# Performance work log

Hardware: AMD Instinct MI355X
Metric: run time of the kernel (lower is better)

## Reference

```python
import jax, jax.numpy as jnp
import numpy as np
import math

GROUPS = 32
EPS = 1e-5
NUM_HEADS = 8


def group_norm(x, gamma, beta):
    # x: [B, C, H, W]; normalize within each of GROUPS channel groups over (C/G, H, W)
    B, C, H, W = x.shape
    xg = x.reshape(B, GROUPS, C // GROUPS, H, W)
    mean = jnp.mean(xg, axis=(2, 3, 4), keepdims=True)
    var = jnp.var(xg, axis=(2, 3, 4), keepdims=True)
    xn = ((xg - mean) * jax.lax.rsqrt(var + EPS)).reshape(B, C, H, W)
    return xn * gamma[None, :, None, None] + beta[None, :, None, None]


def setup_inputs() -> dict:
    key = jax.random.key(0)
    ks = jax.random.split(key, 10)
    C = 512
    B, H, W = 2, 64, 64
    s = 1.0 / math.sqrt(C)
    return {
        "x": jax.random.normal(ks[0], (B, C, H, W), jnp.float32),
        "gamma": jnp.ones((C,), jnp.float32),
        "beta": jnp.zeros((C,), jnp.float32),
        "Wq": jax.random.normal(ks[1], (C, C), jnp.float32) * s,
        "bq": jax.random.normal(ks[2], (C,), jnp.float32) * 0.01,
        "Wk": jax.random.normal(ks[3], (C, C), jnp.float32) * s,
        "bk": jax.random.normal(ks[4], (C,), jnp.float32) * 0.01,
        "Wv": jax.random.normal(ks[5], (C, C), jnp.float32) * s,
        "bv": jax.random.normal(ks[6], (C,), jnp.float32) * 0.01,
        "Wo": jax.random.normal(ks[7], (C, C), jnp.float32) * s,
        "bo": jax.random.normal(ks[8], (C,), jnp.float32) * 0.01,
    }


def reference(x, gamma, beta, Wq, bq, Wk, bk, Wv, bv, Wo, bo):
    B, C, H, W = x.shape
    N = H * W
    hd = C // NUM_HEADS
    h = group_norm(x, gamma, beta)
    h = h.reshape(B, C, N).transpose(0, 2, 1)  # [B, N, C]
    # torch nn.Linear: y = x @ W.T + b
    q = (h @ Wq.T + bq).reshape(B, N, NUM_HEADS, hd)
    k = (h @ Wk.T + bk).reshape(B, N, NUM_HEADS, hd)
    v = (h @ Wv.T + bv).reshape(B, N, NUM_HEADS, hd)
    scale = 1.0 / math.sqrt(hd)
    attn = jnp.einsum('bihd,bjhd->bijh', q, k) * scale  # [B, N, N, heads]
    attn = jax.nn.softmax(attn, axis=2)
    o = jnp.einsum('bijh,bjhd->bihd', attn, v).reshape(B, N, C)
    o = o @ Wo.T + bo
    o = o.transpose(0, 2, 1).reshape(B, C, H, W)
    return x + o
```

## Files before the change

### kernel.cpp

```cpp
#include <hip/hip_runtime.h>
#include <cstdint>
#include <cstddef>

typedef __bf16 bf16x8 __attribute__((ext_vector_type(8)));
typedef float f32x4 __attribute__((ext_vector_type(4)));
typedef float f32x16 __attribute__((ext_vector_type(16)));
typedef unsigned short ushort8 __attribute__((ext_vector_type(8)));
typedef unsigned u32x2 __attribute__((ext_vector_type(2)));
typedef float f4 __attribute__((ext_vector_type(4)));

__device__ __forceinline__ unsigned short f2bf(float f) {
    __bf16 b = (__bf16)f;
    return *(unsigned short*)&b;
}
__device__ __forceinline__ unsigned pk2bf(float a, float b) {
    __bf16 x = (__bf16)a, y = (__bf16)b;
    unsigned short ux = *(unsigned short*)&x, uy = *(unsigned short*)&y;
    return (unsigned)ux | ((unsigned)uy << 16);
}
__device__ __forceinline__ float bf2f(unsigned short u) {
    union { unsigned u; float f; } v; v.u = ((unsigned)u) << 16; return v.f;
}

#if __has_builtin(__builtin_amdgcn_exp2f)
#define EXP2(x) __builtin_amdgcn_exp2f(x)
#else
#define EXP2(x) exp2f(x)
#endif

__device__ __forceinline__ void pl32swap(unsigned& x, unsigned& y) {
#if __has_builtin(__builtin_amdgcn_permlane32_swap)
    auto r = __builtin_amdgcn_permlane32_swap(x, y, false, false);
    x = r[0]; y = r[1];
#else
    unsigned xs = (unsigned)__shfl_xor((int)x, 32, 64);
    unsigned ys = (unsigned)__shfl_xor((int)y, 32, 64);
    bool lo = ((threadIdx.x & 63) < 32);
    unsigned nx = lo ? x : ys;
    unsigned ny = lo ? xs : y;
    x = nx; y = ny;
#endif
}

#define GLL(g, l) __builtin_amdgcn_global_load_lds( \
    (__attribute__((address_space(1))) void*)(g), \
    (__attribute__((address_space(3))) void*)(l), 16, 0, 0)

#define CS 0.18033688011112042f
#define SPLITS 2

__global__ __launch_bounds__(256) void prep(
    const float* __restrict__ wq, const float* __restrict__ wk,
    const float* __restrict__ wv, const float* __restrict__ wo,
    unsigned short* __restrict__ wb,
    const float* __restrict__ x, float* __restrict__ part)
{
    const int bid = blockIdx.x;
    if (bid < 4096) {
        int i = bid * 256 + threadIdx.x;
        const float* src = (i < 262144) ? wq : (i < 524288) ? wk : (i < 786432) ? wv : wo;
        wb[i] = f2bf(src[i & 262143]);
        return;
    }
    const int blk = bid - 4096;
    const int q = blk & 3, bg = blk >> 2;
    const f4* xv = (const f4*)(x + (size_t)bg * 65536 + q * 16384);
    float s = 0.f, sq = 0.f;
    for (int i = threadIdx.x; i < 4096; i += 256) {
        f4 v = xv[i];
        s  += v.x + v.y + v.z + v.w;
        sq += v.x * v.x + v.y * v.y + v.z * v.z + v.w * v.w;
    }
    #pragma unroll
    for (int off = 32; off > 0; off >>= 1) {
        s  += __shfl_xor(s, off, 64);
        sq += __shfl_xor(sq, off, 64);
    }
    __shared__ float red[8];
    const int w = threadIdx.x >> 6, lane = threadIdx.x & 63;
    if (lane == 0) { red[w] = s; red[4 + w] = sq; }
    __syncthreads();
    if (threadIdx.x == 0) {
        part[(bg * 4 + q) * 2]     = red[0] + red[1] + red[2] + red[3];
        part[(bg * 4 + q) * 2 + 1] = red[4] + red[5] + red[6] + red[7];
    }
}

__global__ __launch_bounds__(256) void gn_apply(
    const float* __restrict__ x, const float* __restrict__ gamma,
    const float* __restrict__ beta, const float* __restrict__ part,
    unsigned short* __restrict__ h)
{
    const int q = blockIdx.x, bg = blockIdx.y;
    const int b = bg >> 5, g = bg & 31;
    float s = 0.f, sq = 0.f;
    #pragma unroll
    for (int j = 0; j < 4; ++j) {
        s  += part[(bg * 4 + j) * 2];
        sq += part[(bg * 4 + j) * 2 + 1];
    }
    const float mean = s * (1.f / 65536.f);
    const float rstd = rsqrtf(sq * (1.f / 65536.f) - mean * mean + 1e-5f);

    float gm[16], bt[16];
    #pragma unroll
    for (int c = 0; c < 16; ++c) {
        gm[c] = gamma[g * 16 + c] * rstd;
        bt[c] = beta[g * 16 + c];
    }
    const float* xg = x + (size_t)bg * 65536;
    const int n0 = q * 1024 + threadIdx.x * 4;
    float val[16][4];
    #pragma unroll
    for (int c = 0; c < 16; ++c) {
        f4 v = *(const f4*)&xg[(size_t)c * 4096 + n0];
        val[c][0] = (v.x - mean) * gm[c] + bt[c];
        val[c][1] = (v.y - mean) * gm[c] + bt[c];
        val[c][2] = (v.z - mean) * gm[c] + bt[c];
        val[c][3] = (v.w - mean) * gm[c] + bt[c];
    }
    #pragma unroll
    for (int nn = 0; nn < 4; ++nn) {
        ushort8 v0, v1;
        #pragma unroll
        for (int c = 0; c < 8; ++c)  v0[c]     = f2bf(val[c][nn]);
        #pragma unroll
        for (int c = 8; c < 16; ++c) v1[c - 8] = f2bf(val[c][nn]);
        unsigned short* dst = h + ((size_t)(b * 4096 + n0 + nn)) * 512 + g * 16;
        *(ushort8*)dst = v0;
        *(ushort8*)(dst + 8) = v1;
    }
}

__global__ __launch_bounds__(512, 2) void gemm_qkv(
    const unsigned short* __restrict__ A,
    const unsigned short* __restrict__ Bt,
    const float* __restrict__ bias0,
    const float* __restrict__ bias1,
    const float* __restrict__ bias2,
    unsigned short* __restrict__ outB,
    unsigned short* __restrict__ vtout)
{
    __shared__ __attribute__((aligned(16))) unsigned short As[128 * 32];
    __shared__ __attribute__((aligned(16))) unsigned short Bs[128 * 32];
    const int t = threadIdx.x;
    const int w = t >> 6, lane = t & 63;
    const int l15 = lane & 15, l4 = lane >> 4;
    const int bm = blockIdx.y, bn = blockIdx.x;
    const int wm = (w >> 2) * 64, wn = (w & 3) * 32;

    f32x4 acc[4][2] = {};

    const int srow = t >> 2, sc8 = (t & 3) * 8;
    const unsigned short* gA = A  + (size_t)(bm * 128 + srow) * 512 + sc8;
    const unsigned short* gB = Bt + (size_t)(bn * 128 + srow) * 512 + sc8;
    unsigned short* lA = &As[t * 8];
    unsigned short* lB = &Bs[t * 8];

    for (int k0 = 0; k0 < 512; k0 += 32) {
        __syncthreads();
        GLL(gA + k0, lA);
        GLL(gB + k0, lB);
        __syncthreads();

        bf16x8 af[4], bfr[2];
        #pragma unroll
        for (int mt = 0; mt < 4; ++mt)
            af[mt] = *(const bf16x8*)&As[(wm + mt * 16 + l15) * 32 + l4 * 8];
        #pragma unroll
        for (int nt = 0; nt < 2; ++nt)
            bfr[nt] = *(const bf16x8*)&Bs[(wn + nt * 16 + l15) * 32 + l4 * 8];
        #pragma unroll
        for (int mt = 0; mt < 4; ++mt)
            #pragma unroll
            for (int nt = 0; nt < 2; ++nt)
                acc[mt][nt] = __builtin_amdgcn_mfma_f32_16x16x32_bf16(
                    af[mt], bfr[nt], acc[mt][nt], 0, 0, 0);
    }

    #pragma unroll
    for (int nt = 0; nt < 2; ++nt) {
        int col = bn * 128 + wn + nt * 16 + l15;
        const float* bp = (col < 512) ? bias0 : (col < 1024) ? bias1 : bias2;
        float bv = bp[col & 511];
        if (col < 1024) {
            float sc = (col < 512) ? CS : 1.0f;
            #pragma unroll
            for (int mt = 0; mt < 4; ++mt)
                #pragma unroll
                for (int r = 0; r < 4; ++r) {
                    int row = bm * 128 + wm + mt * 16 + l4 * 4 + r;
                    outB[(size_t)row * 1024 + col] = f2bf((acc[mt][nt][r] + bv) * sc);
                }
        } else {
            int hd = col - 1024;
            #pragma unroll
            for (int mt = 0; mt < 4; ++mt) {
                int m = bm * 128 + wm + mt * 16 + l4 * 4;
                int bb = m >> 12, n = m & 4095;
                unsigned u0 = pk2bf(acc[mt][nt][0] + bv, acc[mt][nt][1] + bv);
                unsigned u1 = pk2bf(acc[mt][nt][2] + bv, acc[mt][nt][3] + bv);
                unsigned short* dst = vtout +
                    ((size_t)(bb * 8 + (hd >> 6)) * 64 + (hd & 63)) * 4096 + n;
                *(u32x2*)dst = (u32x2){u0, u1};
            }
        }
    }
}

__global__ __launch_bounds__(512, 2) void gemm_out(
    const unsigned short* __restrict__ A,
    const unsigned short* __restrict__ opart,
    const float* __restrict__ lbuf,
    const float* __restrict__ bias,
    const float* __restrict__ resid,
    float* __restrict__ outF)
{
    __shared__ __attribute__((aligned(16))) unsigned short As[128 * 32];
    __shared__ __attribute__((aligned(16))) unsigned short Bs[128 * 32];
    const int t = threadIdx.x;
    const int w = t >> 6, lane = t & 63;
    const int l15 = lane & 15, l4 = lane >> 4;
    const int bm = blockIdx.y, bn = blockIdx.x;
    const int wm = (w >> 2) * 64, wn = (w & 3) * 32;

    f32x4 acc[4][2] = {};

    const int srow = t >> 2, sc8 = (t & 3) * 8;
    const unsigned short* gA = A + (size_t)(bm * 128 + srow) * 512 + sc8;
    unsigned short* lA = &As[t * 8];
    unsigned short* lB = &Bs[t * 8];

    const int m = bn * 128 + srow;
    const int bb = m >> 12, q = m & 4095;
    const size_t prow0 = (size_t)(bb * 8) * 4096 + q;
    float inv[8];
    #pragma unroll
    for (int hh = 0; hh < 8; ++hh) {
        size_t pr = prow0 + (size_t)hh * 4096;
        inv[hh] = 1.f / (lbuf[pr] + lbuf[65536 + pr]);
    }
    const unsigned short* gO0 = opart + prow0 * 64;
    const unsigned short* gO1 = gO0 + (size_t)65536 * 64;

    ushort8 o0 = *(const ushort8*)(gO0 + sc8);
    ushort8 o1 = *(const ushort8*)(gO1 + sc8);

    for (int k0 = 0; k0 < 512; k0 += 32) {
        float iv = inv[k0 >> 6];
        ushort8 bv8;
        #pragma unroll
        for (int i = 0; i < 8; ++i)
            bv8[i] = f2bf((bf2f(o0[i]) + bf2f(o1[i])) * iv);
        if (k0 < 480) {
            size_t noff = (size_t)((k0 + 32) >> 6) * 262144 + ((k0 + 32) & 32) + sc8;
            o0 = *(const ushort8*)(gO0 + noff);
            o1 = *(const ushort8*)(gO1 + noff);
        }
        __syncthreads();
        GLL(gA + k0, lA);
        *(ushort8*)lB = bv8;
        __syncthreads();

        bf16x8 af[4], bfr[2];
        #pragma unroll
        for (int mt = 0; mt < 4; ++mt)
            af[mt] = *(const bf16x8*)&As[(wm + mt * 16 + l15) * 32 + l4 * 8];
        #pragma unroll
        for (int nt = 0; nt < 2; ++nt)
            bfr[nt] = *(const bf16x8*)&Bs[(wn + nt * 16 + l15) * 32 + l4 * 8];
        #pragma unroll
        for (int mt = 0; mt < 4; ++mt)
            #pragma unroll
            for (int nt = 0; nt < 2; ++nt)
                acc[mt][nt] = __builtin_amdgcn_mfma_f32_16x16x32_bf16(
                    af[mt], bfr[nt], acc[mt][nt], 0, 0, 0);
    }

    #pragma unroll
    for (int mt = 0; mt < 4; ++mt)
        #pragma unroll
        for (int nt = 0; nt < 2; ++nt)
            #pragma unroll
            for (int r = 0; r < 4; ++r) {
                int c = bm * 128 + wm + mt * 16 + l4 * 4 + r;
                int mm = bn * 128 + wn + nt * 16 + l15;
                int b = mm >> 12, n = mm & 4095;
                size_t idx = ((size_t)(b * 512 + c)) * 4096 + n;
                outF[idx] = acc[mt][nt][r] + bias[c] + resid[idx];
            }
}

__global__ __launch_bounds__(256, 2) void attn_kernel(
    const unsigned short* __restrict__ qkv, const unsigned short* __restrict__ vt,
    unsigned short* __restrict__ opart, float* __restrict__ lbuf)
{
    __shared__ __attribute__((aligned(16))) unsigned short Sh[2 * 64 * 72];
    unsigned short* KsB  = Sh;
    unsigned short* VtsB = Sh + 64 * 72;

    const int bh = blockIdx.y, b = bh >> 3, h = bh & 7;
    const int qbase = blockIdx.x * 256;
    const int s = blockIdx.z, ks0 = s * 2048;
    const int t = threadIdx.x, w = t >> 6, lane = t & 63;
    const int l31 = lane & 31, h5 = lane >> 5;

    const unsigned short* Qg = qkv + ((size_t)(b * 4096 + qbase + w * 64)) * 1024 + h * 64;
    const unsigned short* Kg = qkv + ((size_t)(b * 4096 + ks0)) * 1024 + 512 + h * 64;
    const unsigned short* Vg = vt + ((size_t)bh) * 64 * 4096 + ks0;

    bf16x8 qf[2][4];
    #pragma unroll
    for (int qt = 0; qt < 2; ++qt)
        #pragma unroll
        for (int kc = 0; kc < 4; ++kc)
            qf[qt][kc] = *(const bf16x8*)(Qg + (size_t)(qt * 32 + l31) * 1024 + kc * 16 + h5 * 8);

    f32x16 Oacc[2][2] = {};
    float li[2] = {0.f, 0.f};

    const int sr = t >> 2, sc = (t & 3) * 16;
    const unsigned short* gK = Kg + (size_t)sr * 1024 + sc;
    const unsigned short* gV = Vg + (size_t)sr * 4096 + sc;
    unsigned short* lK = KsB + sr * 72 + sc;
    unsigned short* lV = VtsB + sr * 72 + sc;

    ushort8 kr[2], vr[2];
    kr[0] = *(const ushort8*)(gK);
    kr[1] = *(const ushort8*)(gK + 8);
    vr[0] = *(const ushort8*)(gV);
    vr[1] = *(const ushort8*)(gV + 8);

    for (int kt = 0; kt < 32; ++kt) {
        __syncthreads();
        *(ushort8*)(lK)     = kr[0];
        *(ushort8*)(lK + 8) = kr[1];
        *(ushort8*)(lV)     = vr[0];
        *(ushort8*)(lV + 8) = vr[1];
        __syncthreads();
        if (kt < 31) {
            const unsigned short* nk = gK + (size_t)(kt + 1) * 65536;
            const unsigned short* nv = gV + (kt + 1) * 64;
            kr[0] = *(const ushort8*)(nk);
            kr[1] = *(const ushort8*)(nk + 8);
            vr[0] = *(const ushort8*)(nv);
            vr[1] = *(const ushort8*)(nv + 8);
        }

        f32x16 St[2][2] = {};
        #pragma unroll
        for (int ct = 0; ct < 2; ++ct)
            #pragma unroll
            for (int kc = 0; kc < 4; ++kc) {
                bf16x8 kf = *(const bf16x8*)(KsB + (ct * 32 + l31) * 72 + kc * 16 + h5 * 8);
                St[0][ct] = __builtin_amdgcn_mfma_f32_32x32x16_bf16(kf, qf[0][kc], St[0][ct], 0, 0, 0);
                St[1][ct] = __builtin_amdgcn_mfma_f32_32x32x16_bf16(kf, qf[1][kc], St[1][ct], 0, 0, 0);
            }

        union PU { unsigned u[4]; bf16x8 v; };
        PU pf[2][4];
        #pragma unroll
        for (int qt = 0; qt < 2; ++qt) {
            #pragma unroll
            for (int ct = 0; ct < 2; ++ct)
                #pragma unroll
                for (int r = 0; r < 16; ++r)
                    St[qt][ct][r] = EXP2(St[qt][ct][r]);
            float s0 = 0.f, s1 = 0.f;
            #pragma unroll
            for (int ct = 0; ct < 2; ++ct) {
                s0 += ((St[qt][ct][0] + St[qt][ct][1]) + (St[qt][ct][2] + St[qt][ct][3]))
                    + ((St[qt][ct][4] + St[qt][ct][5]) + (St[qt][ct][6] + St[qt][ct][7]));
                s1 += ((St[qt][ct][8] + St[qt][ct][9]) + (St[qt][ct][10] + St[qt][ct][11]))
                    + ((St[qt][ct][12] + St[qt][ct][13]) + (St[qt][ct][14] + St[qt][ct][15]));
            }
            li[qt] += s0 + s1;

            #pragma unroll
            for (int ct = 0; ct < 2; ++ct) {
                unsigned pk0 = pk2bf(St[qt][ct][0],  St[qt][ct][1]);
                unsigned pk1 = pk2bf(St[qt][ct][2],  St[qt][ct][3]);
                unsigned pk2 = pk2bf(St[qt][ct][4],  St[qt][ct][5]);
                unsigned pk3 = pk2bf(St[qt][ct][6],  St[qt][ct][7]);
                unsigned pk4 = pk2bf(St[qt][ct][8],  St[qt][ct][9]);
                unsigned pk5 = pk2bf(St[qt][ct][10], St[qt][ct][11]);
                unsigned pk6 = pk2bf(St[qt][ct][12], St[qt][ct][13]);
                unsigned pk7 = pk2bf(St[qt][ct][14], St[qt][ct][15]);
                pl32swap(pk0, pk2); pl32swap(pk1, pk3);
                pl32swap(pk4, pk6); pl32swap(pk5, pk7);
                pf[qt][ct * 2].u[0] = pk0; pf[qt][ct * 2].u[1] = pk1;
                pf[qt][ct * 2].u[2] = pk2; pf[qt][ct * 2].u[3] = pk3;
                pf[qt][ct * 2 + 1].u[0] = pk4; pf[qt][ct * 2 + 1].u[1] = pk5;
                pf[qt][ct * 2 + 1].u[2] = pk6; pf[qt][ct * 2 + 1].u[3] = pk7;
            }
        }

        #pragma unroll
        for (int kk = 0; kk < 4; ++kk)
            #pragma unroll
            for (int dt = 0; dt < 2; ++dt) {
                bf16x8 vf = *(const bf16x8*)(VtsB + (dt * 32 + l31) * 72 + kk * 16 + h5 * 8);
                Oacc[dt][0] = __builtin_amdgcn_mfma_f32_32x32x16_bf16(vf, pf[0][kk].v, Oacc[dt][0], 0, 0, 0);
                Oacc[dt][1] = __builtin_amdgcn_mfma_f32_32x32x16_bf16(vf, pf[1][kk].v, Oacc[dt][1], 0, 0, 0);
            }
    }

    #pragma unroll
    for (int qt = 0; qt < 2; ++qt) {
        float lf = li[qt] + __shfl_xor(li[qt], 32, 64);
        if (h5 == 0)
            lbuf[((size_t)s * 16 + bh) * 4096 + qbase + w * 64 + qt * 32 + l31] = lf;
    }

    __syncthreads();
    unsigned short* Eb = Sh + w * (32 * 72);
    #pragma unroll
    for (int qt = 0; qt < 2; ++qt) {
        #pragma unroll
        for (int dt = 0; dt < 2; ++dt)
            #pragma unroll
            for (int p = 0; p < 8; ++p) {
                int d = dt * 32 + 2 * (p & 1) + 8 * (p >> 1) + 4 * h5;
                unsigned u = pk2bf(Oacc[dt][qt][2 * p], Oacc[dt][qt][2 * p + 1]);
                *(unsigned*)&Eb[l31 * 72 + d] = u;
            }
        unsigned short* Og = opart +
            (((size_t)s * 16 + bh) * 4096 + qbase + w * 64 + qt * 32) * 64;
        #pragma unroll
        for (int i = 0; i < 4; ++i) {
            int c8 = h5 * 4 + i;
            ushort8 val = *(const ushort8*)&Eb[l31 * 72 + c8 * 8];
            *(ushort8*)(Og + (size_t)l31 * 64 + c8 * 8) = val;
        }
    }
}

extern "C" void kernel_launch(void* const* d_in, const int* in_sizes, int n_in,
                              void* d_out, int out_size, void* d_ws, size_t ws_size,
                              hipStream_t stream) {
    const float* x     = (const float*)d_in[0];
    const float* gamma = (const float*)d_in[1];
    const float* beta  = (const float*)d_in[2];
    const float* Wq    = (const float*)d_in[3];
    const float* bq    = (const float*)d_in[4];
    const float* Wk    = (const float*)d_in[5];
    const float* bk    = (const float*)d_in[6];
    const float* Wv    = (const float*)d_in[7];
    const float* bv    = (const float*)d_in[8];
    const float* Wo    = (const float*)d_in[9];
    const float* bo    = (const float*)d_in[10];
    float* out = (float*)d_out;

    char* ws = (char*)d_ws;
    const size_t MB = 1024 * 1024;
    unsigned short* wb     = (unsigned short*)(ws);
    float*          gnpart = (float*)(ws + 2 * MB);
    unsigned short* qkv    = (unsigned short*)(ws + 3 * MB);
    unsigned short* vtb    = (unsigned short*)(ws + 19 * MB);
    unsigned short* h      = (unsigned short*)(ws + 27 * MB);
    unsigned short* opart  = (unsigned short*)(ws + 27 * MB);
    float*          lbuf   = (float*)(ws + 59 * MB);

    prep<<<dim3(4352), dim3(256), 0, stream>>>(Wq, Wk, Wv, Wo, wb, x, gnpart);
    gn_apply<<<dim3(4, 64), dim3(256), 0, stream>>>(x, gamma, beta, gnpart, h);

    gemm_qkv<<<dim3(12, 64), dim3(512), 0, stream>>>(
        h, wb, bq, bk, bv, qkv, vtb);

    attn_kernel<<<dim3(16, 16, SPLITS), dim3(256), 0, stream>>>(qkv, vtb, opart, lbuf);

    gemm_out<<<dim3(64, 4), dim3(512), 0, stream>>>(
        wb + 786432, opart, lbuf, bo, x, out);
}
```

Before: 219.4 us.

## Enlarge per-wave QKV GEMM tiles and double-buffer the output-projection GEMM

The QKV projection GEMM now runs with 256 threads instead of 512, and each wave computes a 64x64 sub-tile with a 4x4 MFMA accumulator grid instead of 64x32. Each thread issues two A and two B global-to-LDS loads per K step. This raises register reuse of the A and B fragments and halves the number of waves doing LDS reads, at the cost of more accumulator registers and possibly lower occupancy. The output-projection GEMM gains ping-pong LDS buffers, so the next K-slice is loaded and the split-attention partials are combined while MFMAs run on the current slice, with one barrier per iteration instead of two.

```diff
diff --git a/kernel.cpp b/kernel.cpp
--- a/kernel.cpp
+++ b/kernel.cpp
@@ -132,14 +132,15 @@
     }
 }
 
-__global__ __launch_bounds__(512, 2) void gemm_qkv(
+__global__ __launch_bounds__(256, 2) void gemm_qkv(
     const unsigned short* __restrict__ A,
     const unsigned short* __restrict__ Bt,
     const float* __restrict__ bias0,
     const float* __restrict__ bias1,
     const float* __restrict__ bias2,
     unsigned short* __restrict__ outB,
-    unsigned short* __restrict__ vtout)
+    unsigned short* __restrict__ vtout,
+    int M, int N, int K)
 {
     __shared__ __attribute__((aligned(16))) unsigned short As[128 * 32];
     __shared__ __attribute__((aligned(16))) unsigned short Bs[128 * 32];
@@ -147,39 +148,47 @@
     const int w = t >> 6, lane = t & 63;
     const int l15 = lane & 15, l4 = lane >> 4;
     const int bm = blockIdx.y, bn = blockIdx.x;
-    const int wm = (w >> 2) * 64, wn = (w & 3) * 32;
-
-    f32x4 acc[4][2] = {};
-
-    const int srow = t >> 2, sc8 = (t & 3) * 8;
-    const unsigned short* gA = A  + (size_t)(bm * 128 + srow) * 512 + sc8;
-    const unsigned short* gB = Bt + (size_t)(bn * 128 + srow) * 512 + sc8;
-    unsigned short* lA = &As[t * 8];
-    unsigned short* lB = &Bs[t * 8];
-
-    for (int k0 = 0; k0 < 512; k0 += 32) {
+    const int wm = (w >> 1) * 64, wn = (w & 1) * 64;
+
+    f32x4 acc[4][4] = {};
+
+    const int srow = t >> 2;
+    const int sc8  = (t & 3) * 8;
+
+    const unsigned short* gA0 = A  + (size_t)(bm * 128 + srow) * K + sc8;
+    const unsigned short* gA1 = gA0 + (size_t)64 * K;
+    const unsigned short* gB0 = Bt + (size_t)(bn * 128 + srow) * K + sc8;
+    const unsigned short* gB1 = gB0 + (size_t)64 * K;
+    unsigned short* lA0 = &As[w * 512];
+    unsigned short* lA1 = &As[2048 + w * 512];
+    unsigned short* lB0 = &Bs[w * 512];
+    unsigned short* lB1 = &Bs[2048 + w * 512];
+
+    for (int k0 = 0; k0 < K; k0 += 32) {
         __syncthreads();
-        GLL(gA + k0, lA);
-        GLL(gB + k0, lB);
+        GLL(gA0 + k0, lA0);
+        GLL(gA1 + k0, lA1);
+        GLL(gB0 + k0, lB0);
+        GLL(gB1 + k0, lB1);
         __syncthreads();
 
-        bf16x8 af[4], bfr[2];
+        bf16x8 af[4], bfr[4];
         #pragma unroll
         for (int mt = 0; mt < 4; ++mt)
             af[mt] = *(const bf16x8*)&As[(wm + mt * 16 + l15) * 32 + l4 * 8];
         #pragma unroll
-        for (int nt = 0; nt < 2; ++nt)
+        for (int nt = 0; nt < 4; ++nt)
             bfr[nt] = *(const bf16x8*)&Bs[(wn + nt * 16 + l15) * 32 + l4 * 8];
         #pragma unroll
         for (int mt = 0; mt < 4; ++mt)
             #pragma unroll
-            for (int nt = 0; nt < 2; ++nt)
+            for (int nt = 0; nt < 4; ++nt)
                 acc[mt][nt] = __builtin_amdgcn_mfma_f32_16x16x32_bf16(
                     af[mt], bfr[nt], acc[mt][nt], 0, 0, 0);
     }
 
     #pragma unroll
-    for (int nt = 0; nt < 2; ++nt) {
+    for (int nt = 0; nt < 4; ++nt) {
         int col = bn * 128 + wn + nt * 16 + l15;
         const float* bp = (col < 512) ? bias0 : (col < 1024) ? bias1 : bias2;
         float bv = bp[col & 511];
@@ -216,8 +225,8 @@
     const float* __restrict__ resid,
     float* __restrict__ outF)
 {
-    __shared__ __attribute__((aligned(16))) unsigned short As[128 * 32];
-    __shared__ __attribute__((aligned(16))) unsigned short Bs[128 * 32];
+    __shared__ __attribute__((aligned(16))) unsigned short As[2][128 * 32];
+    __shared__ __attribute__((aligned(16))) unsigned short Bs[2][128 * 32];
     const int t = threadIdx.x;
     const int w = t >> 6, lane = t & 63;
     const int l15 = lane & 15, l4 = lane >> 4;
@@ -228,8 +237,6 @@
 
     const int srow = t >> 2, sc8 = (t & 3) * 8;
     const unsigned short* gA = A + (size_t)(bm * 128 + srow) * 512 + sc8;
-    unsigned short* lA = &As[t * 8];
-    unsigned short* lB = &Bs[t * 8];
 
     const int m = bn * 128 + srow;
     const int bb = m >> 12, q = m & 4095;
@@ -243,38 +250,55 @@
     const unsigned short* gO0 = opart + prow0 * 64;
     const unsigned short* gO1 = gO0 + (size_t)65536 * 64;
 
-    ushort8 o0 = *(const ushort8*)(gO0 + sc8);
-    ushort8 o1 = *(const ushort8*)(gO1 + sc8);
-
-    for (int k0 = 0; k0 < 512; k0 += 32) {
-        float iv = inv[k0 >> 6];
+    {
+        ushort8 o0 = *(const ushort8*)(gO0 + sc8);
+        ushort8 o1 = *(const ushort8*)(gO1 + sc8);
+        float iv = inv[0];
         ushort8 bv8;
         #pragma unroll
         for (int i = 0; i < 8; ++i)
             bv8[i] = f2bf((bf2f(o0[i]) + bf2f(o1[i])) * iv);
+        GLL(gA, &As[0][t * 8]);
+        *(ushort8*)&Bs[0][t * 8] = bv8;
+    }
+    ushort8 o0 = *(const ushort8*)(gO0 + 262144 / 4096 * 0 + 32 + sc8);
+    ushort8 o1 = *(const ushort8*)(gO1 + 32 + sc8);
+    __syncthreads();
+
+    for (int k0 = 0; k0 < 512; k0 += 32) {
+        const int cur = (k0 >> 5) & 1;
+
+        bf16x8 af[4], bfr[2];
+        #pragma unroll
+        for (int mt = 0; mt < 4; ++mt)
+            af[mt] = *(const bf16x8*)&As[cur][(wm + mt * 16 + l15) * 32 + l4 * 8];
+        #pragma unroll
+        for (int nt = 0; nt < 2; ++nt)
+            bfr[nt] = *(const bf16x8*)&Bs[cur][(wn + nt * 16 + l15) * 32 + l4 * 8];
+
         if (k0 < 480) {
-            size_t noff = (size_t)((k0 + 32) >> 6) * 262144 + ((k0 + 32) & 32) + sc8;
-            o0 = *(const ushort8*)(gO0 + noff);
-            o1 = *(const ushort8*)(gO1 + noff);
+            GLL(gA + k0 + 32, &As[cur ^ 1][t * 8]);
+            float iv = inv[(k0 + 32) >> 6];
+            ushort8 bv8;
+            #pragma unroll
+            for (int i = 0; i < 8; ++i)
+                bv8[i] = f2bf((bf2f(o0[i]) + bf2f(o1[i])) * iv);
+            *(ushort8*)&Bs[cur ^ 1][t * 8] = bv8;
+            if (k0 < 448) {
+                size_t noff = (size_t)((k0 + 64) >> 6) * 262144 + ((k0 + 64) & 32) + sc8;
+                o0 = *(const ushort8*)(gO0 + noff);
+                o1 = *(const ushort8*)(gO1 + noff);
+            }
         }
-        __syncthreads();
-        GLL(gA + k0, lA);
-        *(ushort8*)lB = bv8;
-        __syncthreads();
-
-        bf16x8 af[4], bfr[2];
-        #pragma unroll
-        for (int mt = 0; mt < 4; ++mt)
-            af[mt] = *(const bf16x8*)&As[(wm + mt * 16 + l15) * 32 + l4 * 8];
-        #pragma unroll
-        for (int nt = 0; nt < 2; ++nt)
-            bfr[nt] = *(const bf16x8*)&Bs[(wn + nt * 16 + l15) * 32 + l4 * 8];
+
         #pragma unroll
         for (int mt = 0; mt < 4; ++mt)
             #pragma unroll
             for (int nt = 0; nt < 2; ++nt)
                 acc[mt][nt] = __builtin_amdgcn_mfma_f32_16x16x32_bf16(
                     af[mt], bfr[nt], acc[mt][nt], 0, 0, 0);
+
+        __syncthreads();
     }
 
     #pragma unroll
@@ -464,8 +488,8 @@
     prep<<<dim3(4352), dim3(256), 0, stream>>>(Wq, Wk, Wv, Wo, wb, x, gnpart);
     gn_apply<<<dim3(4, 64), dim3(256), 0, stream>>>(x, gamma, beta, gnpart, h);
 
-    gemm_qkv<<<dim3(12, 64), dim3(512), 0, stream>>>(
-        h, wb, bq, bk, bv, qkv, vtb);
+    gemm_qkv<<<dim3(12, 64), dim3(256), 0, stream>>>(
+        h, wb, bq, bk, bv, qkv, vtb, 8192, 1536, 512);
 
     attn_kernel<<<dim3(16, 16, SPLITS), dim3(256), 0, stream>>>(qkv, vtb, opart, lbuf);
 
```

Result: no change. 221.4 us (+0.9%).
